# Kernel optimization log

Measured on AMD Instinct MI355X. Metric: run time of the kernel, lower is better.

Reference implementation:

```python
import jax, jax.numpy as jnp
import numpy as np

DIM = 64
HEADS = 16
HEAD_DIM = DIM // HEADS  # 4
CHUNK = 128
LN_EPS = 1e-5


def _ln(v, w, b):
    mu = jnp.mean(v, axis=-1, keepdims=True)
    var = jnp.var(v, axis=-1, keepdims=True)
    return (v - mu) * jax.lax.rsqrt(var + LN_EPS) * w + b


def setup_inputs() -> dict:
    key = jax.random.key(0)
    ks = jax.random.split(key, 16)
    B, C, H, W = 8, 64, 128, 128
    s = 0.02
    inp = {
        "x": jax.random.normal(ks[0], (B, C, H, W), jnp.float32),
        "text_embed": jax.random.normal(ks[1], (B, C, H, W), jnp.float32),
        # Linear weights stored as [in, out] (torch uses [out, in]; math identical via x @ W)
        "q_w": jax.random.normal(ks[2], (DIM, DIM), jnp.float32) * s,
        "q_b": jnp.zeros((DIM,), jnp.float32),
        "k_w": jax.random.normal(ks[3], (DIM, DIM), jnp.float32) * s,
        "k_b": jnp.zeros((DIM,), jnp.float32),
        "v_w": jax.random.normal(ks[4], (DIM, DIM), jnp.float32) * s,
        "v_b": jnp.zeros((DIM,), jnp.float32),
        "o_w": jax.random.normal(ks[5], (DIM, DIM), jnp.float32) * s,
        "o_b": jnp.zeros((DIM,), jnp.float32),
        "ln1_w": jnp.ones((DIM,), jnp.float32),
        "ln1_b": jnp.zeros((DIM,), jnp.float32),
        "ln2_w": jnp.ones((DIM,), jnp.float32),
        "ln2_b": jnp.zeros((DIM,), jnp.float32),
        "fc1_w": jax.random.normal(ks[6], (DIM, 4 * DIM), jnp.float32) * s,
        "fc1_b": jnp.zeros((4 * DIM,), jnp.float32),
        "fc2_w": jax.random.normal(ks[7], (4 * DIM, DIM), jnp.float32) * s,
        "fc2_b": jnp.zeros((DIM,), jnp.float32),
        # 1x1 conv as [out_ch, in_ch]
        "conv_w": jax.random.normal(ks[8], (DIM, DIM), jnp.float32) * s,
        "conv_b": jnp.zeros((DIM,), jnp.float32),
        # FiLM MLP: pooled_channels=64*4*4=1024 -> 128 -> 128
        "m1_w": jax.random.normal(ks[9], (1024, 2 * DIM), jnp.float32) * s,
        "m1_b": jnp.zeros((2 * DIM,), jnp.float32),
        "m2_w": jax.random.normal(ks[10], (2 * DIM, 2 * DIM), jnp.float32) * s,
        "m2_b": jnp.zeros((2 * DIM,), jnp.float32),
    }
    return inp


def reference(x, text_embed, q_w, q_b, k_w, k_b, v_w, v_b, o_w, o_b,
              ln1_w, ln1_b, ln2_w, ln2_b, fc1_w, fc1_b, fc2_w, fc2_b,
              conv_w, conv_b, m1_w, m1_b, m2_w, m2_b):
    B, C, H, W = x.shape
    N = H * W
    Nc = N // CHUNK  # number of local chunks (block-diagonal attention)
    scale = jnp.sqrt(jnp.float32(HEAD_DIM))

    prior_flat = text_embed.reshape(B, C, N).transpose(0, 2, 1)  # [B,N,C]
    x_flat = x.reshape(B, C, N).transpose(0, 2, 1)               # [B,N,C]

    prior_norm = _ln(prior_flat, ln1_w, ln1_b)
    Q = prior_norm @ q_w + q_b
    K = x_flat @ k_w + k_b
    V = x_flat @ v_w + v_b

    # blocked heads: [B, Nc, CHUNK, HEADS, HEAD_DIM]
    Qb = Q.reshape(B, Nc, CHUNK, HEADS, HEAD_DIM)
    Kb = K.reshape(B, Nc, CHUNK, HEADS, HEAD_DIM)
    Vb = V.reshape(B, Nc, CHUNK, HEADS, HEAD_DIM)

    scores = jnp.einsum('bnqhd,bnkhd->bnhqk', Qb, Kb) / scale  # [B,Nc,H,CHUNK,CHUNK]
    probs = jax.nn.softmax(scores, axis=-1)
    attn = jnp.einsum('bnhqk,bnkhd->bnqhd', probs, Vb).reshape(B, N, DIM)

    attn = attn @ o_w + o_b
    h = attn + prior_flat
    h_norm = _ln(h, ln2_w, ln2_b)
    ffn = jax.nn.gelu(h_norm @ fc1_w + fc1_b, approximate=False) @ fc2_w + fc2_b
    h = ffn + h

    h4 = h.transpose(0, 2, 1).reshape(B, DIM, H, W)
    conv = jnp.einsum('bihw,oi->bohw', h4, conv_w) + conv_b[None, :, None, None]
    out = conv + x  # TIAM output

    # FiLM: adaptive_avg_pool2d to (4,4) (H,W divisible by 4)
    te = text_embed.reshape(B, C, 4, H // 4, 4, W // 4).mean(axis=(3, 5))  # [B,C,4,4]
    te = te.reshape(B, -1)  # [B, 1024]
    hmlp = jax.nn.leaky_relu(te @ m1_w + m1_b, negative_slope=0.01)
    gb = hmlp @ m2_w + m2_b  # [B, 128]
    gamma = gb[:, :DIM][:, :, None, None]
    beta = gb[:, DIM:][:, :, None, None]
    return (1.0 + gamma) * out + beta
```

## Files before the change

kernel.cpp:

```cpp
#include <hip/hip_runtime.h>
#include <hip/hip_bf16.h>

#define NB 8
#define NTOK 16384
#define TOTTOK (NB*NTOK)

typedef __hip_bfloat16 bf16;
typedef __attribute__((ext_vector_type(8))) short bfrag;
typedef __attribute__((ext_vector_type(4))) float ffrag;

#define MFMA(a,b,c) __builtin_amdgcn_mfma_f32_16x16x32_bf16(a,b,c,0,0,0)

__device__ __forceinline__ float b2f(bf16 v){ return __bfloat162float(v); }
__device__ __forceinline__ bf16 f2b(float v){ return __float2bfloat16(v); }
__device__ __forceinline__ float bfu(unsigned short u){
    union { float f; unsigned v; } x; x.v = ((unsigned)u) << 16; return x.f; }
__device__ __forceinline__ unsigned short bu(bf16 b){
    union { bf16 b; unsigned short u; } x; x.b = b; return x.u; }
__device__ __forceinline__ void ld4(const bf16* p, float* f){
    uint2 r = *(const uint2*)p;
    f[0]=bfu(r.x & 0xffff); f[1]=bfu(r.x >> 16); f[2]=bfu(r.y & 0xffff); f[3]=bfu(r.y >> 16);
}
__device__ __forceinline__ float fastrcp(float x){
    float r; asm("v_rcp_f32 %0, %1" : "=v"(r) : "v"(x)); return r; }
__device__ __forceinline__ unsigned cvtpk(float lo, float hi){
    unsigned r; asm("v_cvt_pk_bf16_f32 %0,%1,%2" : "=v"(r) : "v"(lo), "v"(hi)); return r; }
__device__ __forceinline__ void stb(bf16* p, float v){
    unsigned r; asm("v_cvt_pk_bf16_f32 %0,%1,%1" : "=v"(r) : "v"(v));
    *(unsigned short*)p = (unsigned short)r; }
__device__ __forceinline__ float gelu_t(float x){
    float x2 = x*x;
    float y  = x * fmaf(x2, 0.1029425f, 2.3022077f);
    float z  = exp2f(y);
    float rc = fastrcp(z + 1.f);
    return x - x*rc;
}
__device__ __forceinline__ bfrag ld_frag(const bf16* p, int stride){
    int lane = threadIdx.x & 63;
    return *(const bfrag*)(p + (lane & 15)*stride + (lane >> 4)*8);
}

#define WI_QKV   0
#define WI_OW    13824
#define WI_CW    18432
#define WI_W1    23040
#define WI_W2    41472
#define WI_CONST 57856
#define WI_TOT   58752

__global__ __launch_bounds__(256) void wprep_kernel(
    const float* __restrict__ qw, const float* __restrict__ kw, const float* __restrict__ vw,
    const float* __restrict__ ow, const float* __restrict__ cw,
    const float* __restrict__ w1, const float* __restrict__ w2,
    const float* __restrict__ ln1w, const float* __restrict__ ln1b,
    const float* __restrict__ qb, const float* __restrict__ kb_, const float* __restrict__ vb,
    const float* __restrict__ ob, const float* __restrict__ ln2w, const float* __restrict__ ln2b,
    const float* __restrict__ b1, const float* __restrict__ b2, const float* __restrict__ cb,
    bf16* __restrict__ WI)
{
    int gid = blockIdx.x*256 + threadIdx.x;
    if (gid >= WI_TOT) return;
    float v = 0.f;
    if (gid < WI_OW){
        int m = gid / 4608, r = gid % 4608;
        int o = r / 72, ii = r % 72;
        const float* src = (m==0)? qw : (m==1)? kw : vw;
        if (ii < 64) v = src[ii*64 + o];
    } else if (gid < WI_CW){
        int r = gid - WI_OW;
        int o = r / 72, ii = r % 72;
        if (ii < 64) v = ow[ii*64 + o];
    } else if (gid < WI_W1){
        int r = gid - WI_CW;
        int co = r / 72, ii = r % 72;
        if (ii < 64) v = cw[co*64 + ii];
    } else if (gid < WI_W2){
        int r = gid - WI_W1;
        int gg = r / 2304, rr = r % 2304;
        int ol = rr / 72, ii = rr % 72;
        if (ii < 64) v = w1[ii*256 + gg*32 + ol];
    } else if (gid < WI_CONST){
        int a = gid - WI_W2;
        int o = a >> 8, ra = a & 255;
        int blk = ra >> 3, wi = ra & 7;
        int k = ((blk ^ (o & 7)) << 3) | wi;
        v = w2[k*64 + o];
    } else {
        int r = gid - WI_CONST;
        if      (r <  64) v = ln1w[r];
        else if (r < 128) v = ln1b[r-64];
        else if (r < 192) v = qb[r-128];
        else if (r < 256) v = kb_[r-192];
        else if (r < 320) v = vb[r-256];
        else if (r < 384) v = ob[r-320];
        else if (r < 448) v = ln2w[r-384];
        else if (r < 512) v = ln2b[r-448];
        else if (r < 768) v = b1[r-512];
        else if (r < 832) v = b2[r-768];
        else              v = cb[r-832];
    }
    WI[gid] = f2b(v);
}

__global__ __launch_bounds__(256) void pool_kernel(const float* __restrict__ te,
                                                   float* __restrict__ pool)
{
    int blk = blockIdx.x;
    const float* src = te + (size_t)blk * NTOK;
    int tid = threadIdx.x;
    __shared__ float R[16];
    if (tid < 16) R[tid] = 0.f;
    __syncthreads();
    int rw = (tid >> 3) & 3;
    float acc[4] = {0.f, 0.f, 0.f, 0.f};
    #pragma unroll
    for (int u = 0; u < 16; ++u){
        float4 v = *(const float4*)(src + u*1024 + tid*4);
        acc[u >> 2] += v.x + v.y + v.z + v.w;
    }
    #pragma unroll
    for (int rh = 0; rh < 4; ++rh) atomicAdd(&R[rh*4 + rw], acc[rh]);
    __syncthreads();
    if (tid < 16) pool[blk*16 + tid] = R[tid];
}

__global__ __launch_bounds__(128) void film_kernel(const float* __restrict__ pool,
        const float* __restrict__ m1w, const float* __restrict__ m1b,
        const float* __restrict__ m2w, const float* __restrict__ m2b,
        float* __restrict__ gb){
    int b = blockIdx.x; int j = threadIdx.x;
    __shared__ float tel[1024];
    __shared__ float hm[128];
    for (int i = j; i < 1024; i += 128) tel[i] = pool[b*1024 + i] * (1.f/1024.f);
    __syncthreads();
    float s = m1b[j];
    for (int i = 0; i < 1024; ++i) s = fmaf(tel[i], m1w[i*128 + j], s);
    hm[j] = (s > 0.f) ? s : 0.01f*s;
    __syncthreads();
    float g = m2b[j];
    for (int i = 0; i < 128; ++i) g = fmaf(hm[i], m2w[i*128 + j], g);
    gb[b*128 + j] = g;
}

#define OFF_TE2 0
#define OFF_XT  16384
#define OFF_PN  34816
#define OFF_WT  53248
#define OFF_W2T 47616
#define OFF_CON 80896
#define SCALE_Q 0.72134752044448170f

__device__ __forceinline__ void ln_phase(const bf16* S, bf16* D,
                                         const bf16* Wt, const bf16* Bs, int tid)
{
    int tok = tid >> 2, q4 = tid & 3;
    float vals[16];
    int op2[2];
    float s = 0.f, s2 = 0.f;
    #pragma unroll
    for (int u8 = 0; u8 < 2; ++u8){
        int o = (q4*2 + u8) ^ (tok & 7);
        op2[u8] = o;
        uint4 v = *(const uint4*)(S + tok*64 + o*8);
        const unsigned* ap = &v.x;
        float* vp = vals + u8*8;
        #pragma unroll
        for (int e = 0; e < 4; ++e){
            float lo = bfu(ap[e] & 0xffff), hi = bfu(ap[e] >> 16);
            vp[e*2] = lo; vp[e*2+1] = hi;
            s += lo + hi;
            s2 = fmaf(lo, lo, fmaf(hi, hi, s2));
        }
    }
    s  += __shfl_xor(s, 1, 64);  s2 += __shfl_xor(s2, 1, 64);
    s  += __shfl_xor(s, 2, 64);  s2 += __shfl_xor(s2, 2, 64);
    float mean = s * (1.f/64.f);
    float var  = s2 * (1.f/64.f) - mean*mean;
    float rstd = rsqrtf(var + 1e-5f);
    #pragma unroll
    for (int u8 = 0; u8 < 2; ++u8){
        int cc0 = op2[u8]*8;
        uint4 wv = *(const uint4*)(Wt + cc0);
        uint4 bv = *(const uint4*)(Bs + cc0);
        const unsigned* wp = &wv.x;
        const unsigned* bp = &bv.x;
        uint4 o; unsigned* opp = &o.x;
        #pragma unroll
        for (int e = 0; e < 4; ++e){
            float lo = (vals[u8*8+e*2]  -mean)*rstd*bfu(wp[e] & 0xffff) + bfu(bp[e] & 0xffff);
            float hi = (vals[u8*8+e*2+1]-mean)*rstd*bfu(wp[e] >> 16)    + bfu(bp[e] >> 16);
            opp[e] = cvtpk(lo, hi);
        }
        *(uint4*)(D + tok*72 + cc0) = o;
    }
}

__global__ __launch_bounds__(512,4) void mega_kernel(
    const float* __restrict__ x, const float* __restrict__ te,
    const bf16* __restrict__ WI, const float* __restrict__ gb, float* __restrict__ out)
{
    __shared__ __align__(16) char sm[81920];
    bf16* TE2 = (bf16*)(sm + OFF_TE2);
    bf16* XT  = (bf16*)(sm + OFF_XT);
    bf16* PN  = (bf16*)(sm + OFF_PN);
    bf16* WT  = (bf16*)(sm + OFF_WT);
    bf16* VT  = (bf16*)(sm + OFF_WT);
    bf16* OWT = (bf16*)(sm + OFF_WT);
    bf16* W1S = (bf16*)(sm + OFF_PN);
    bf16* P   = (bf16*)(sm + OFF_PN + 4608);
    bf16* CWs = (bf16*)(sm + OFF_PN);
    bf16* W2T = (bf16*)(sm + OFF_W2T);
    bf16* CON = (bf16*)(sm + OFF_CON);
    bf16* OT  = (bf16*)(sm + OFF_TE2);

    int tid = threadIdx.x;
    int w = tid >> 6, lane = tid & 63;
    int g = lane >> 4, c = lane & 15;
    int t0g = blockIdx.x * 128;
    int b = t0g >> 14, n0 = t0g & (NTOK-1);
    const ffrag fz = {0.f,0.f,0.f,0.f};

    {
        bf16* Tx = PN;
        bf16* Tt = WT;
        if (tid < 16) ((uint4*)CON)[tid] = ((const uint4*)(WI + WI_CONST))[tid];
        int c0 = tid >> 3, j16 = (tid & 7) * 16;
        const float* xp = x  + (size_t)b*64*NTOK + (size_t)c0*NTOK + n0 + j16;
        const float* tp = te + (size_t)b*64*NTOK + (size_t)c0*NTOK + n0 + j16;
        float4 a0 = *(const float4*)(xp);
        float4 a1 = *(const float4*)(xp + 4);
        float4 a2 = *(const float4*)(xp + 8);
        float4 a3 = *(const float4*)(xp + 12);
        float4 e0 = *(const float4*)(tp);
        float4 e1 = *(const float4*)(tp + 4);
        float4 e2 = *(const float4*)(tp + 8);
        float4 e3 = *(const float4*)(tp + 12);
        uint4 o0, o1;
        o0.x = cvtpk(a0.x, a0.y); o0.y = cvtpk(a0.z, a0.w);
        o0.z = cvtpk(a1.x, a1.y); o0.w = cvtpk(a1.z, a1.w);
        o1.x = cvtpk(a2.x, a2.y); o1.y = cvtpk(a2.z, a2.w);
        o1.z = cvtpk(a3.x, a3.y); o1.w = cvtpk(a3.z, a3.w);
        *(uint4*)(Tx + c0*136 + j16)     = o0;
        *(uint4*)(Tx + c0*136 + j16 + 8) = o1;
        o0.x = cvtpk(e0.x, e0.y); o0.y = cvtpk(e0.z, e0.w);
        o0.z = cvtpk(e1.x, e1.y); o0.w = cvtpk(e1.z, e1.w);
        o1.x = cvtpk(e2.x, e2.y); o1.y = cvtpk(e2.z, e2.w);
        o1.z = cvtpk(e3.x, e3.y); o1.w = cvtpk(e3.z, e3.w);
        *(uint4*)(Tt + c0*136 + j16)     = o0;
        *(uint4*)(Tt + c0*136 + j16 + 8) = o1;
        __syncthreads();
        #pragma unroll
        for (int p = 0; p < 2; ++p){
            int idx = p*512 + tid;
            int tok = idx & 127, seg = idx >> 7;
            const bf16* rx = Tx + seg*1088 + tok;
            const bf16* rt = Tt + seg*1088 + tok;
            uint4 ox, ot;
            ox.x = (unsigned)bu(rx[0])   | ((unsigned)bu(rx[136]) << 16);
            ox.y = (unsigned)bu(rx[272]) | ((unsigned)bu(rx[408]) << 16);
            ox.z = (unsigned)bu(rx[544]) | ((unsigned)bu(rx[680]) << 16);
            ox.w = (unsigned)bu(rx[816]) | ((unsigned)bu(rx[952]) << 16);
            *(uint4*)(XT + tok*72 + seg*8) = ox;
            ot.x = (unsigned)bu(rt[0])   | ((unsigned)bu(rt[136]) << 16);
            ot.y = (unsigned)bu(rt[272]) | ((unsigned)bu(rt[408]) << 16);
            ot.z = (unsigned)bu(rt[544]) | ((unsigned)bu(rt[680]) << 16);
            ot.w = (unsigned)bu(rt[952-136]) | ((unsigned)bu(rt[952]) << 16);
            *(uint4*)(TE2 + tok*64 + seg*8) = ot;
        }
    }
    __syncthreads();
    {
        ln_phase(TE2, PN, CON, CON + 64, tid);
        const uint4* wq = (const uint4*)(WI + WI_QKV);
        for (int i = tid; i < 1728; i += 512) ((uint4*)WT)[i] = wq[i];
    }
    __syncthreads();
    {
        if (tid < 24) ((uint4*)CON)[tid] = ((const uint4*)(WI + WI_CONST + 128))[tid];
        ffrag accQ[4], accK[4], accV[4];
        #pragma unroll
        for (int nt=0;nt<4;++nt){ accQ[nt]=fz; accK[nt]=fz; accV[nt]=fz; }
        bfrag aQ[2], aX[2];
        #pragma unroll
        for (int k2=0;k2<2;++k2){
            aQ[k2] = ld_frag(PN + (w*16)*72 + k2*32, 72);
            aX[k2] = ld_frag(XT + (w*16)*72 + k2*32, 72);
        }
        for (int nt = 0; nt < 4; ++nt){
            #pragma unroll
            for (int k2 = 0; k2 < 2; ++k2){
                bfrag bq2 = ld_frag(WT +        nt*16*72 + k2*32, 72);
                bfrag bk2 = ld_frag(WT + 4608 + nt*16*72 + k2*32, 72);
                bfrag bv2 = ld_frag(WT + 9216 + nt*16*72 + k2*32, 72);
                accQ[nt] = MFMA(aQ[k2], bq2, accQ[nt]);
                accK[nt] = MFMA(aX[k2], bk2, accK[nt]);
                accV[nt] = MFMA(aX[k2], bv2, accV[nt]);
            }
        }
        __syncthreads();
        int rq = g*4;
        #pragma unroll
        for (int nt=0;nt<4;++nt){
            int n = nt*16 + c;
            float bq3 = b2f(CON[n]), bk3 = b2f(CON[64+n]), bv3 = b2f(CON[128+n]);
            #pragma unroll
            for (int r=0;r<4;++r){
                int m = w*16 + rq + r;
                stb(PN + m*72 + n, (accQ[nt][r] + bq3) * SCALE_Q);
                stb(XT + m*72 + n, accK[nt][r] + bk3);
                int kp = ((m >> 6) << 6) + (m & 15)*4 + ((m >> 4) & 3);
                stb(VT + (5*(n>>2) + (n&3))*136 + kp, accV[nt][r] + bv3);
            }
        }
        if (tid < 256){
            int row = 5*(tid >> 4) + 4, col8 = (tid & 15)*8;
            uint4 ov; ov.x = ov.y = ov.z = ov.w = 0x3f803f80u;
            *(uint4*)(VT + row*136 + col8) = ov;
        }
    }
    __syncthreads();
    {
        bfrag bq[8];
        #pragma unroll
        for (int nt = 0; nt < 8; ++nt) bq[nt] = ld_frag(XT + nt*16*72 + (w>>2)*32, 72);
        __syncthreads();
        bf16* Pw = XT + w*1024;
        #pragma unroll 1
        for (int hh = 0; hh < 2; ++hh){
            int h = w*2 + hh;
            int ag = w & 3;
            bfrag bv4[4];
            #pragma unroll
            for (int kk = 0; kk < 4; ++kk)
                bv4[kk] = ld_frag(VT + (5*h)*136 + (kk>>1)*64 + (kk&1)*32, 136);
            #pragma unroll 2
            for (int qt = 0; qt < 8; ++qt){
                int q = qt*16 + c;
                uint2 qv = *(const uint2*)(PN + q*72 + h*4);
                union { bfrag f; uint2 u[2]; } A;
                uint2 z2; z2.x = 0u; z2.y = 0u;
                uint2 sel = (g == ag) ? qv : z2;
                if (hh){ A.u[0] = z2;  A.u[1] = sel; }
                else   { A.u[0] = sel; A.u[1] = z2;  }
                ffrag og = fz;
                #pragma unroll
                for (int kh = 0; kh < 2; ++kh){
                    ffrag acc[4];
                    #pragma unroll
                    for (int nt = 0; nt < 4; ++nt) acc[nt] = MFMA(A.f, bq[kh*4+nt], fz);
                    #pragma unroll
                    for (int nt = 0; nt < 4; ++nt){
                        #pragma unroll
                        for (int r = 0; r < 4; ++r) acc[nt][r] = exp2f(acc[nt][r]);
                    }
                    #pragma unroll
                    for (int r = 0; r < 4; ++r){
                        uint2 pk;
                        pk.x = cvtpk(acc[0][r], acc[1][r]);
                        pk.y = cvtpk(acc[2][r], acc[3][r]);
                        int row = 4*g + r;
                        *(uint2*)(Pw + row*64 + (((c>>1) ^ (row&7)) << 3) + ((c&1) << 2)) = pk;
                    }
                    #pragma unroll
                    for (int ks = 0; ks < 2; ++ks){
                        bfrag ap = *(const bfrag*)(Pw + c*64 + (((ks*4 + g) ^ (c&7)) << 3));
                        og = MFMA(ap, bv4[kh*2 + ks], og);
                    }
                }
                #pragma unroll
                for (int r = 0; r < 4; ++r){
                    float lr = __shfl(og[r], (lane & 48) | 4, 64);
                    if (c < 4)
                        stb(PN + (qt*16 + 4*g + r)*72 + h*4 + c, og[r] * fastrcp(lr));
                }
            }
        }
    }
    __syncthreads();
    {
        const uint4* oi = (const uint4*)(WI + WI_OW);
        for (int i = tid; i < 576; i += 512) ((uint4*)OWT)[i] = oi[i];
        if (tid < 24) ((uint4*)CON)[tid] = ((const uint4*)(WI + WI_CONST + 320))[tid];
        __syncthreads();
        ffrag acc2[4];
        #pragma unroll
        for (int nt=0;nt<4;++nt) acc2[nt] = fz;
        bfrag af2[2];
        #pragma unroll
        for (int k2=0;k2<2;++k2)
            af2[k2] = ld_frag(PN + (w*16)*72 + k2*32, 72);
        #pragma unroll
        for (int nt=0;nt<4;++nt){
            #pragma unroll
            for (int k2=0;k2<2;++k2){
                bfrag bf_ = ld_frag(OWT + nt*16*72 + k2*32, 72);
                acc2[nt] = MFMA(af2[k2], bf_, acc2[nt]);
            }
        }
        int rq = g*4;
        #pragma unroll
        for (int nt=0;nt<4;++nt){
            int n = nt*16 + c;
            float bo = b2f(CON[n]);
            #pragma unroll
            for (int r=0;r<4;++r){
                int m = w*16 + rq + r;
                stb(TE2 + m*64 + n, acc2[nt][r] + bo + b2f(TE2[m*64 + n]));
            }
        }
    }
    __syncthreads();
    ln_phase(TE2, XT, CON + 64, CON + 128, tid);
    __syncthreads();
    {
        const uint4* w2i = (const uint4*)(WI + WI_W2);
        for (int i = tid; i < 2048; i += 512) ((uint4*)W2T)[i] = w2i[i];
        if (tid < 48) ((uint4*)CON)[tid] = ((const uint4*)(WI + WI_CONST + 512))[tid];
        bfrag af[2];
        #pragma unroll
        for (int k2=0;k2<2;++k2)
            af[k2] = ld_frag(XT + (w*16)*72 + k2*32, 72);
        ffrag acc2[4];
        #pragma unroll
        for (int nt=0;nt<4;++nt) acc2[nt] = fz;
        int rq = g*4;
        const uint4* w1i = (const uint4*)(WI + WI_W1);
        uint4 pA;
        if (tid < 288) pA = w1i[tid];
        for (int gg = 0; gg < 8; ++gg){
            __syncthreads();
            if (tid < 288){
                ((uint4*)W1S)[tid] = pA;
                if (gg < 7) pA = w1i[(gg+1)*288 + tid];
            }
            __syncthreads();
            ffrag accg[2];
            #pragma unroll
            for (int ntl=0;ntl<2;++ntl) accg[ntl] = fz;
            #pragma unroll
            for (int ntl=0;ntl<2;++ntl){
                #pragma unroll
                for (int k2=0;k2<2;++k2){
                    bfrag bf_ = ld_frag(W1S + ntl*16*72 + k2*32, 72);
                    accg[ntl] = MFMA(af[k2], bf_, accg[ntl]);
                }
            }
            #pragma unroll
            for (int ntl=0;ntl<2;++ntl){
                int n = ntl*16 + c;
                float bb = b2f(CON[gg*32 + n]);
                #pragma unroll
                for (int r=0;r<4;++r){
                    int m = w*16 + rq + r;
                    float xv = accg[ntl][r] + bb;
                    stb(P + m*32 + ((((n>>3) ^ ((m>>1)&3)) << 3) | (n & 7)), gelu_t(xv));
                }
            }
            {
                int rr = w*16 + c;
                bfrag ap = *(const bfrag*)(P + rr*32 + ((g ^ ((rr>>1)&3)) << 3));
                #pragma unroll
                for (int nt=0;nt<4;++nt){
                    int n = nt*16 + c;
                    int chunk = gg*4 + g;
                    bfrag bf2 = *(const bfrag*)(W2T + n*256 + ((chunk ^ (n&7)) << 3));
                    acc2[nt] = MFMA(ap, bf2, acc2[nt]);
                }
            }
        }
        #pragma unroll
        for (int nt=0;nt<4;++nt){
            int n = nt*16 + c;
            float bb = b2f(CON[256+n]);
            #pragma unroll
            for (int r=0;r<4;++r){
                int m = w*16 + rq + r;
                stb(XT + m*72 + n, acc2[nt][r] + bb + b2f(TE2[m*64 + n]));
            }
        }
    }
    __syncthreads();
    {
        const uint4* ci = (const uint4*)(WI + WI_CW);
        for (int i = tid; i < 576; i += 512) ((uint4*)CWs)[i] = ci[i];
        __syncthreads();
        bfrag ac[2];
        #pragma unroll
        for (int k2=0;k2<2;++k2) ac[k2] = ld_frag(CWs + ((w&3)*16)*72 + k2*32, 72);
        int rq = g*4;
        #pragma unroll
        for (int nt4 = 0; nt4 < 4; ++nt4){
            int nt = (w>>2)*4 + nt4;
            ffrag accc = fz;
            #pragma unroll
            for (int k2=0;k2<2;++k2){
                bfrag bh = ld_frag(XT + nt*16*72 + k2*32, 72);
                accc = MFMA(ac[k2], bh, accc);
            }
            int tok = nt*16 + c;
            #pragma unroll
            for (int r=0;r<4;++r){
                int co = (w&3)*16 + rq + r;
                stb(OT + co*128 + tok, accc[r] + b2f(CON[320+co]));
            }
        }
    }
    __syncthreads();
    {
        int cc = tid >> 3, seg = (tid & 7)*16;
        float gamma = 1.f + gb[b*128 + cc];
        float beta  = gb[b*128 + 64 + cc];
        const size_t gbase = (size_t)b*64*NTOK + (size_t)cc*NTOK + n0 + seg;
        #pragma unroll
        for (int u = 0; u < 4; ++u){
            float cv[4];
            ld4(OT + cc*128 + seg + u*4, cv);
            float4 xv = *(const float4*)(x + gbase + u*4);
            float4 ov;
            ov.x = fmaf(gamma, cv[0]+xv.x, beta);
            ov.y = fmaf(gamma, cv[1]+xv.y, beta);
            ov.z = fmaf(gamma, cv[2]+xv.z, beta);
            ov.w = fmaf(gamma, cv[3]+xv.w, beta);
            *(float4*)(out + gbase + u*4) = ov;
        }
    }
}

extern "C" void kernel_launch(void* const* d_in, const int* in_sizes, int n_in,
                              void* d_out, int out_size, void* d_ws, size_t ws_size,
                              hipStream_t stream){
    const float* x   = (const float*)d_in[0];
    const float* te  = (const float*)d_in[1];
    const float* qw  = (const float*)d_in[2];
    const float* qb  = (const float*)d_in[3];
    const float* kw  = (const float*)d_in[4];
    const float* kb  = (const float*)d_in[5];
    const float* vw  = (const float*)d_in[6];
    const float* vb  = (const float*)d_in[7];
    const float* ow  = (const float*)d_in[8];
    const float* ob  = (const float*)d_in[9];
    const float* ln1w= (const float*)d_in[10];
    const float* ln1b= (const float*)d_in[11];
    const float* ln2w= (const float*)d_in[12];
    const float* ln2b= (const float*)d_in[13];
    const float* w1  = (const float*)d_in[14];
    const float* b1  = (const float*)d_in[15];
    const float* w2  = (const float*)d_in[16];
    const float* b2  = (const float*)d_in[17];
    const float* cw  = (const float*)d_in[18];
    const float* cb  = (const float*)d_in[19];
    const float* m1w = (const float*)d_in[20];
    const float* m1b = (const float*)d_in[21];
    const float* m2w = (const float*)d_in[22];
    const float* m2b = (const float*)d_in[23];

    char* ws = (char*)d_ws;
    float* pool = (float*)(ws);
    float* gbp  = (float*)(ws + 32768);
    bf16* WI    = (bf16*)(ws + 36864);

    wprep_kernel<<<(WI_TOT + 255)/256, 256, 0, stream>>>(
        qw, kw, vw, ow, cw, w1, w2,
        ln1w, ln1b, qb, kb, vb, ob, ln2w, ln2b, b1, b2, cb, WI);
    pool_kernel<<<NB*64, 256, 0, stream>>>(te, pool);
    film_kernel<<<NB, 128, 0, stream>>>(pool, m1w, m1b, m2w, m2b, gbp);
    mega_kernel<<<TOTTOK/128, 512, 0, stream>>>(x, te, WI, gbp, (float*)d_out);
}
```

Measured before the change: 285.8 us.

## Double-buffer FC1 weights, overlap weight loads with LN, add MFMA priority hints

Adds s_setprio around MFMA sections so waves issuing matrix ops get scheduler priority. It double-buffers the per-group fc1 weight tile into an alternate shared-memory region (W1X), which drops one barrier per loop iteration. The fc2 weight and conv weight global loads are issued into registers before LN and before the FFN epilogue, hiding their latency, and two barriers are removed. This raises register pressure and depends on W1X not overlapping live data in XT.

```diff
diff --git a/kernel.cpp b/kernel.cpp
--- a/kernel.cpp
+++ b/kernel.cpp
@@ -207,6 +207,7 @@
     bf16* VT  = (bf16*)(sm + OFF_WT);
     bf16* OWT = (bf16*)(sm + OFF_WT);
     bf16* W1S = (bf16*)(sm + OFF_PN);
+    bf16* W1X = (bf16*)(sm + OFF_XT) + 4608;
     bf16* P   = (bf16*)(sm + OFF_PN + 4608);
     bf16* CWs = (bf16*)(sm + OFF_PN);
     bf16* W2T = (bf16*)(sm + OFF_W2T);
@@ -286,6 +287,7 @@
             aQ[k2] = ld_frag(PN + (w*16)*72 + k2*32, 72);
             aX[k2] = ld_frag(XT + (w*16)*72 + k2*32, 72);
         }
+        __builtin_amdgcn_s_setprio(1);
         for (int nt = 0; nt < 4; ++nt){
             #pragma unroll
             for (int k2 = 0; k2 < 2; ++k2){
@@ -297,6 +299,7 @@
                 accV[nt] = MFMA(aX[k2], bv2, accV[nt]);
             }
         }
+        __builtin_amdgcn_s_setprio(0);
         __syncthreads();
         int rq = g*4;
         #pragma unroll
@@ -346,8 +349,10 @@
                 #pragma unroll
                 for (int kh = 0; kh < 2; ++kh){
                     ffrag acc[4];
+                    __builtin_amdgcn_s_setprio(1);
                     #pragma unroll
                     for (int nt = 0; nt < 4; ++nt) acc[nt] = MFMA(A.f, bq[kh*4+nt], fz);
+                    __builtin_amdgcn_s_setprio(0);
                     #pragma unroll
                     for (int nt = 0; nt < 4; ++nt){
                         #pragma unroll
@@ -361,11 +366,13 @@
                         int row = 4*g + r;
                         *(uint2*)(Pw + row*64 + (((c>>1) ^ (row&7)) << 3) + ((c&1) << 2)) = pk;
                     }
+                    __builtin_amdgcn_s_setprio(1);
                     #pragma unroll
                     for (int ks = 0; ks < 2; ++ks){
                         bfrag ap = *(const bfrag*)(Pw + c*64 + (((ks*4 + g) ^ (c&7)) << 3));
                         og = MFMA(ap, bv4[kh*2 + ks], og);
                     }
+                    __builtin_amdgcn_s_setprio(0);
                 }
                 #pragma unroll
                 for (int r = 0; r < 4; ++r){
@@ -389,6 +396,7 @@
         #pragma unroll
         for (int k2=0;k2<2;++k2)
             af2[k2] = ld_frag(PN + (w*16)*72 + k2*32, 72);
+        __builtin_amdgcn_s_setprio(1);
         #pragma unroll
         for (int nt=0;nt<4;++nt){
             #pragma unroll
@@ -397,6 +405,7 @@
                 acc2[nt] = MFMA(af2[k2], bf_, acc2[nt]);
             }
         }
+        __builtin_amdgcn_s_setprio(0);
         int rq = g*4;
         #pragma unroll
         for (int nt=0;nt<4;++nt){
@@ -410,11 +419,20 @@
         }
     }
     __syncthreads();
-    ln_phase(TE2, XT, CON + 64, CON + 128, tid);
-    __syncthreads();
     {
         const uint4* w2i = (const uint4*)(WI + WI_W2);
-        for (int i = tid; i < 2048; i += 512) ((uint4*)W2T)[i] = w2i[i];
+        uint4 w2r0 = w2i[tid];
+        uint4 w2r1 = w2i[512 + tid];
+        uint4 w2r2 = w2i[1024 + tid];
+        uint4 w2r3 = w2i[1536 + tid];
+        ln_phase(TE2, XT, CON + 64, CON + 128, tid);
+        ((uint4*)W2T)[tid]        = w2r0;
+        ((uint4*)W2T)[512 + tid]  = w2r1;
+        ((uint4*)W2T)[1024 + tid] = w2r2;
+        ((uint4*)W2T)[1536 + tid] = w2r3;
+    }
+    __syncthreads();
+    {
         if (tid < 48) ((uint4*)CON)[tid] = ((const uint4*)(WI + WI_CONST + 512))[tid];
         bfrag af[2];
         #pragma unroll
@@ -428,23 +446,25 @@
         uint4 pA;
         if (tid < 288) pA = w1i[tid];
         for (int gg = 0; gg < 8; ++gg){
-            __syncthreads();
+            bf16* Wb = (gg & 1) ? W1X : W1S;
             if (tid < 288){
-                ((uint4*)W1S)[tid] = pA;
+                ((uint4*)Wb)[tid] = pA;
                 if (gg < 7) pA = w1i[(gg+1)*288 + tid];
             }
             __syncthreads();
             ffrag accg[2];
             #pragma unroll
             for (int ntl=0;ntl<2;++ntl) accg[ntl] = fz;
+            __builtin_amdgcn_s_setprio(1);
             #pragma unroll
             for (int ntl=0;ntl<2;++ntl){
                 #pragma unroll
                 for (int k2=0;k2<2;++k2){
-                    bfrag bf_ = ld_frag(W1S + ntl*16*72 + k2*32, 72);
+                    bfrag bf_ = ld_frag(Wb + ntl*16*72 + k2*32, 72);
                     accg[ntl] = MFMA(af[k2], bf_, accg[ntl]);
                 }
             }
+            __builtin_amdgcn_s_setprio(0);
             #pragma unroll
             for (int ntl=0;ntl<2;++ntl){
                 int n = ntl*16 + c;
@@ -459,6 +479,7 @@
             {
                 int rr = w*16 + c;
                 bfrag ap = *(const bfrag*)(P + rr*32 + ((g ^ ((rr>>1)&3)) << 3));
+                __builtin_amdgcn_s_setprio(1);
                 #pragma unroll
                 for (int nt=0;nt<4;++nt){
                     int n = nt*16 + c;
@@ -466,8 +487,14 @@
                     bfrag bf2 = *(const bfrag*)(W2T + n*256 + ((chunk ^ (n&7)) << 3));
                     acc2[nt] = MFMA(ap, bf2, acc2[nt]);
                 }
-            }
-        }
+                __builtin_amdgcn_s_setprio(0);
+            }
+        }
+        const uint4* ci = (const uint4*)(WI + WI_CW);
+        uint4 cw0 = ci[tid];
+        uint4 cw1 = cw0;
+        if (tid < 64) cw1 = ci[512 + tid];
+        __syncthreads();
         #pragma unroll
         for (int nt=0;nt<4;++nt){
             int n = nt*16 + c;
@@ -478,12 +505,11 @@
                 stb(XT + m*72 + n, acc2[nt][r] + bb + b2f(TE2[m*64 + n]));
             }
         }
-    }
-    __syncthreads();
-    {
-        const uint4* ci = (const uint4*)(WI + WI_CW);
-        for (int i = tid; i < 576; i += 512) ((uint4*)CWs)[i] = ci[i];
-        __syncthreads();
+        ((uint4*)CWs)[tid] = cw0;
+        if (tid < 64) ((uint4*)CWs)[512 + tid] = cw1;
+    }
+    __syncthreads();
+    {
         bfrag ac[2];
         #pragma unroll
         for (int k2=0;k2<2;++k2) ac[k2] = ld_frag(CWs + ((w&3)*16)*72 + k2*32, 72);
@@ -492,11 +518,13 @@
         for (int nt4 = 0; nt4 < 4; ++nt4){
             int nt = (w>>2)*4 + nt4;
             ffrag accc = fz;
+            __builtin_amdgcn_s_setprio(1);
             #pragma unroll
             for (int k2=0;k2<2;++k2){
                 bfrag bh = ld_frag(XT + nt*16*72 + k2*32, 72);
                 accc = MFMA(ac[k2], bh, accc);
             }
+            __builtin_amdgcn_s_setprio(0);
             int tok = nt*16 + c;
             #pragma unroll
             for (int r=0;r<4;++r){
```

New measurement: 284.8 us, median of 2. About the same (-0.3%).
